# Performance work log

Measured on AMD Instinct MI355X. Metric: run time of the kernel, lower is better.

## Reference

```python
import jax, jax.numpy as jnp
import numpy as np

B, S, D = 4, 512, 2048
N_HEADS, N_KV, HEAD_DIM = 16, 4, 128
N_REP = N_HEADS // N_KV
FFN = 5632
E, TOPK, R = 8, 2, 16
LORA_SCALE = 32.0 / R  # alpha / r
EPS = 1e-5


def setup_inputs() -> dict:
    key = jax.random.key(0)
    ks = jax.random.split(key, 32)

    def p(k, shape, s=0.02):
        return jax.random.normal(k, shape, jnp.float32) * s

    data = jax.random.normal(ks[0], (B, S, D), jnp.float32)
    # causal additive mask [1,1,S,S]
    causal = jnp.tril(jnp.ones((S, S), jnp.bool_))
    mask = jnp.where(causal, 0.0, -1e9).astype(jnp.float32)[None, None]
    # rotary angles (llama interleaved pairing), half head_dim
    inv_freq = 1.0 / (10000.0 ** (np.arange(0, HEAD_DIM, 2, dtype=np.float32) / HEAD_DIM))
    angles = jnp.asarray(np.arange(S, dtype=np.float32)[:, None] * inv_freq[None, :])
    rope_cos = jnp.cos(angles)  # [S, HEAD_DIM//2]
    rope_sin = jnp.sin(angles)

    inp = dict(
        data=data, mask=mask, rope_cos=rope_cos, rope_sin=rope_sin,
        att_norm_w=jnp.ones((D,), jnp.float32),
        ffn_norm_w=jnp.ones((D,), jnp.float32),
        wq=p(ks[1], (D, D)), wk=p(ks[2], (N_KV * HEAD_DIM, D)),
        wv=p(ks[3], (N_KV * HEAD_DIM, D)), wo=p(ks[4], (D, D)),
        lqA=p(ks[5], (R, D)), lqB=p(ks[6], (D, R)),
        lkA=p(ks[7], (R, D)), lkB=p(ks[8], (N_KV * HEAD_DIM, R)),
        lvA=p(ks[9], (R, D)), lvB=p(ks[10], (N_KV * HEAD_DIM, R)),
        loA=p(ks[11], (R, D)), loB=p(ks[12], (D, R)),
        w1=p(ks[13], (FFN, D)), w2=p(ks[14], (D, FFN)), w3=p(ks[15], (FFN, D)),
        gate_w=p(ks[16], (E, D)),
        eA1=p(ks[17], (E, R, D)), eB1=p(ks[18], (E, FFN, R)),
        eA2=p(ks[19], (E, R, FFN)), eB2=p(ks[20], (E, D, R)),
        eA3=p(ks[21], (E, R, D)), eB3=p(ks[22], (E, FFN, R)),
    )
    return inp


def rmsnorm(x, w):
    return x * jax.lax.rsqrt(jnp.mean(x * x, axis=-1, keepdims=True) + EPS) * w


def lora_linear(x, W, A, Bm):
    # torch Linear weight is [out, in]; lora: x @ A^T @ B^T * scale
    return x @ W.T + ((x @ A.T) @ Bm.T) * LORA_SCALE


def apply_rope(x, cos, sin):
    # x: [B,S,H,Dh]; interleaved complex rotation per pair
    x1, x2 = x[..., 0::2], x[..., 1::2]
    c = cos[None, :, None, :]
    s = sin[None, :, None, :]
    o1 = x1 * c - x2 * s
    o2 = x1 * s + x2 * c
    return jnp.stack([o1, o2], axis=-1).reshape(x.shape)


def transformer_fwd(data, mask, rope_cos, rope_sin, att_norm_w, ffn_norm_w,
                    wq, wk, wv, wo, lqA, lqB, lkA, lkB, lvA, lvB, loA, loB,
                    w1, w2, w3, gate_w, eA1, eB1, eA2, eB2, eA3, eB3):
    b, s, _ = data.shape
    h = rmsnorm(data, att_norm_w)
    xq = lora_linear(h, wq, lqA, lqB).reshape(b, s, N_HEADS, HEAD_DIM)
    xk = lora_linear(h, wk, lkA, lkB).reshape(b, s, N_KV, HEAD_DIM)
    xv = lora_linear(h, wv, lvA, lvB).reshape(b, s, N_KV, HEAD_DIM)
    xq = apply_rope(xq, rope_cos, rope_sin)
    xk = apply_rope(xk, rope_cos, rope_sin)
    # repeat_kv: each kv head repeated n_rep times consecutively
    xk = jnp.repeat(xk, N_REP, axis=2)
    xv = jnp.repeat(xv, N_REP, axis=2)
    scores = jnp.einsum('bshd,bthd->bhst', xq, xk) / jnp.sqrt(jnp.float32(HEAD_DIM))
    scores = scores + mask
    attn = jax.nn.softmax(scores, axis=-1)
    out = jnp.einsum('bhst,bthd->bshd', attn, xv).reshape(b, s, D)
    data = data + lora_linear(out, wo, loA, loB)

    # MoE FFN (MixLoRA): shared base w1/w2/w3 + per-expert LoRA, top-k routing
    hn = rmsnorm(data, ffn_norm_w)
    x = hn.reshape(b * s, D)
    logits = x @ gate_w.T                       # [T, E]
    probs = jax.nn.softmax(logits, axis=-1)
    vals, idx = jax.lax.top_k(probs, TOPK)      # [T, k]
    vals = vals / jnp.sum(vals, axis=-1, keepdims=True)
    T = b * s
    route = jnp.zeros((T, E), x.dtype).at[jnp.arange(T)[:, None], idx].set(vals)
    h1 = x @ w1.T   # shared base projections
    h3 = x @ w3.T
    acc = jnp.zeros((T, D), x.dtype)
    for e in range(E):
        g1 = h1 + ((x @ eA1[e].T) @ eB1[e].T) * LORA_SCALE
        g3 = h3 + ((x @ eA3[e].T) @ eB3[e].T) * LORA_SCALE
        gh = jax.nn.silu(g1) * g3
        oe = gh @ w2.T + ((gh @ eA2[e].T) @ eB2[e].T) * LORA_SCALE
        acc = acc + route[:, e:e + 1] * oe
    return data + acc.reshape(b, s, D)


def reference(data, mask, rope_cos, rope_sin, att_norm_w, ffn_norm_w,
              wq, wk, wv, wo, lqA, lqB, lkA, lkB, lvA, lvB, loA, loB,
              w1, w2, w3, gate_w, eA1, eB1, eA2, eB2, eA3, eB3):
    return transformer_fwd(data, mask, rope_cos, rope_sin, att_norm_w, ffn_norm_w,
                           wq, wk, wv, wo, lqA, lqB, lkA, lkB, lvA, lvB, loA, loB,
                           w1, w2, w3, gate_w, eA1, eB1, eA2, eB2, eA3, eB3)
```

## Files before the change

### kernel.cpp

```cpp
#include <hip/hip_runtime.h>
#include <stdint.h>

#define DI static __device__ __forceinline__

typedef __attribute__((ext_vector_type(8))) short bf16x8;
typedef __attribute__((ext_vector_type(4))) float floatx4;

DI unsigned short f2bf(float x){
  unsigned int u = __float_as_uint(x);
  u += 0x7fffu + ((u >> 16) & 1u);
  return (unsigned short)(u >> 16);
}
DI float bf2f(unsigned short h){ return __uint_as_float(((unsigned int)h) << 16); }

#define GLOAD16(gp, lp) \
  __builtin_amdgcn_global_load_lds((const __attribute__((address_space(1))) unsigned int*)(gp), \
                                   (__attribute__((address_space(3))) unsigned int*)(lp), 16, 0, 0)

#define WAITVM0 asm volatile("s_waitcnt vmcnt(0)" ::: "memory")

template<int OUTM, int RESM, bool CSKIP, bool SPLIT>
__global__ __launch_bounds__(256, 2)
void k_gemm(const unsigned short* __restrict__ A, long lda, long sA1, long sA2, long aLo,
            const unsigned short* __restrict__ B, long ldb, long sB1, long sB2, long bLo,
            void* __restrict__ C, long ldc, long sC1, long sC2, long cLo,
            const void* __restrict__ Rz, long ldr,
            const unsigned short* __restrict__ G1p, const float* __restrict__ ewp, int slot,
            int kIters, int zshift, int bshift)
{
  if (CSKIP && blockIdx.y > blockIdx.x) return;
  __shared__ __attribute__((aligned(16))) unsigned short As[SPLIT ? 8192 : 4096];
  __shared__ __attribute__((aligned(16))) unsigned short Bs[SPLIT ? 8192 : 4096];
  const int tid = threadIdx.x;
  const int w = tid >> 6, lane = tid & 63;
  const int wm = (w >> 1) * 64, wn = (w & 1) * 64;
  const int z = blockIdx.z;
  const int zr = z & ((1 << zshift) - 1);
  const int zb = z >> zshift;
  long k0 = 0;
  if (OUTM == 2 || OUTM == 8) k0 = (long)zb * (long)kIters * 32;
  const unsigned short* Ab = A + (long)((OUTM==8)?0:zb) * sA2 + (long)zr * sA1 + (long)blockIdx.x * 128 * lda + k0;
  const unsigned short* Bb = B + (long)((OUTM==8)?0:zb) * sB2 + (long)(zr >> bshift) * sB1 + (long)blockIdx.y * 128 * ldb + k0;

  const int rlo = w * 16 + (lane & 15);
  const int rhi = 64 + rlo;
  const int cc  = (lane >> 4) * 8;
  unsigned short* ldsA0 = As + w * 512;
  unsigned short* ldsA1 = As + 2048 + w * 512;
  unsigned short* ldsB0 = Bs + w * 512;
  unsigned short* ldsB1 = Bs + 2048 + w * 512;

  floatx4 acc[4][4];
  floatx4 zv = {0.f, 0.f, 0.f, 0.f};
#pragma unroll
  for (int i = 0; i < 4; ++i)
#pragma unroll
    for (int j = 0; j < 4; ++j) acc[i][j] = zv;

  const int abase = (wm >> 4) * 512 + lane * 8;
  const int bbase = (wn >> 4) * 512 + lane * 8;

  for (int kt = 0; kt < kIters; ++kt) {
    const unsigned short* pa = Ab + (long)kt * 32;
    const unsigned short* pb = Bb + (long)kt * 32;
    GLOAD16(pa + (long)rlo * lda + cc, ldsA0);
    GLOAD16(pa + (long)rhi * lda + cc, ldsA1);
    GLOAD16(pb + (long)rlo * ldb + cc, ldsB0);
    GLOAD16(pb + (long)rhi * ldb + cc, ldsB1);
    if (SPLIT) {
      const unsigned short* pal = pa + aLo;
      const unsigned short* pbl = pb + bLo;
      GLOAD16(pal + (long)rlo * lda + cc, As + 4096 + w * 512);
      GLOAD16(pal + (long)rhi * lda + cc, As + 6144 + w * 512);
      GLOAD16(pbl + (long)rlo * ldb + cc, Bs + 4096 + w * 512);
      GLOAD16(pbl + (long)rhi * ldb + cc, Bs + 6144 + w * 512);
    }
    __syncthreads();
    bf16x8 af[4], bfr[4];
#pragma unroll
    for (int i = 0; i < 4; ++i)
      af[i] = *(const bf16x8*)(As + abase + i * 512);
#pragma unroll
    for (int j = 0; j < 4; ++j)
      bfr[j] = *(const bf16x8*)(Bs + bbase + j * 512);
    if (SPLIT) {
      bf16x8 al[4], bl[4];
#pragma unroll
      for (int i = 0; i < 4; ++i)
        al[i] = *(const bf16x8*)(As + 4096 + abase + i * 512);
#pragma unroll
      for (int j = 0; j < 4; ++j)
        bl[j] = *(const bf16x8*)(Bs + 4096 + bbase + j * 512);
#pragma unroll
      for (int i = 0; i < 4; ++i)
#pragma unroll
        for (int j = 0; j < 4; ++j) {
          acc[i][j] = __builtin_amdgcn_mfma_f32_16x16x32_bf16(af[i], bfr[j], acc[i][j], 0, 0, 0);
          acc[i][j] = __builtin_amdgcn_mfma_f32_16x16x32_bf16(af[i], bl[j], acc[i][j], 0, 0, 0);
          acc[i][j] = __builtin_amdgcn_mfma_f32_16x16x32_bf16(al[i], bfr[j], acc[i][j], 0, 0, 0);
        }
    } else {
#pragma unroll
      for (int i = 0; i < 4; ++i)
#pragma unroll
        for (int j = 0; j < 4; ++j)
          acc[i][j] = __builtin_amdgcn_mfma_f32_16x16x32_bf16(af[i], bfr[j], acc[i][j], 0, 0, 0);
    }
    __syncthreads();
  }

  const long mb = (long)blockIdx.x * 128 + wm + ((lane >> 4) * 4);
  const long nb = (long)blockIdx.y * 128 + wn + (lane & 15);
  const long cbase = (long)zb * sC2 + (long)zr * sC1;
#pragma unroll
  for (int i = 0; i < 4; ++i) {
#pragma unroll
    for (int j = 0; j < 4; ++j) {
#pragma unroll
      for (int rr = 0; rr < 4; ++rr) {
        long m = mb + i * 16 + rr;
        long n = nb + j * 16;
        float v = acc[i][j][rr];
        if (RESM == 1) v += ((const float*)Rz)[m * ldr + n];
        if (RESM == 2) v += bf2f(((const unsigned short*)Rz)[m * ldr + n]);
        if (OUTM == 0 || OUTM == 8) ((float*)C)[cbase + m * ldc + n] = v;
        else if (OUTM == 1) ((unsigned short*)C)[cbase + m * ldc + n] = f2bf(v);
        else if (OUTM == 2) atomicAdd((float*)C + cbase + m * ldc + n, v);
        else if (OUTM == 4) {
          float g1 = bf2f(G1p[m * ldc + n]);
          float s1 = g1 / (1.f + __expf(-g1));
          ((unsigned short*)C)[cbase + m * ldc + n] = f2bf(ewp[m * 2 + slot] * s1 * v);
        } else if (OUTM == 5) {
          unsigned short h = f2bf(v);
          unsigned short l = f2bf(v - bf2f(h));
          ((unsigned short*)C)[cbase + m * ldc + n] = h;
          ((unsigned short*)C)[cbase + m * ldc + n + cLo] = l;
        } else {
          long bq = m >> 9, sI = m & 511, kv = n >> 7, dI = n & 127;
          long t = (((bq * 4 + kv) * 128 + dI) << 9) + sI;
          unsigned short h = f2bf(v);
          unsigned short l = f2bf(v - bf2f(h));
          ((unsigned short*)C)[t] = h;
          ((unsigned short*)C)[t + cLo] = l;
        }
      }
    }
  }
}

template<int BM, int BN, bool SPLIT, int OUTM, int DEPTH>
__global__ __launch_bounds__(512, 2)
void k_gemm2(const unsigned short* __restrict__ A, long lda, long aLo,
             const unsigned short* __restrict__ B, long ldb, long bLo,
             void* __restrict__ C, long ldc, long sC2, int kIters)
{
  constexpr int ASZ = BM * 32 * (SPLIT ? 2 : 1);
  constexpr int BSZ = BN * 32 * (SPLIT ? 2 : 1);
  constexpr int TSZ = ASZ + BSZ;
  constexpr int FM = BM / 32, FN = BN / 64;
  __shared__ __attribute__((aligned(16))) unsigned short sm[DEPTH * TSZ];

  const int tid = threadIdx.x;
  const int w = tid >> 6, lane = tid & 63;
  const int wm = (w >> 2) * (BM / 2), wn = (w & 3) * (BN / 4);
  const int zb = blockIdx.z;
  const long k0 = (OUTM == 8) ? (long)zb * (long)kIters * 32 : 0;
  const unsigned short* Ab = A + (long)blockIdx.x * BM * lda + k0;
  const unsigned short* Bb = B + (long)blockIdx.y * BN * ldb + k0;
  const int rA = lane & 15;
  const int cc = (lane >> 4) * 8;

  floatx4 acc[FM][FN];
  floatx4 zv = {0.f, 0.f, 0.f, 0.f};
#pragma unroll
  for (int i = 0; i < FM; ++i)
#pragma unroll
    for (int j = 0; j < FN; ++j) acc[i][j] = zv;

  auto stage = [&](int kt) {
    const unsigned short* pa = Ab + (long)kt * 32;
    const unsigned short* pb = Bb + (long)kt * 32;
    unsigned short* sa = sm + (size_t)(kt & (DEPTH - 1)) * TSZ;
    unsigned short* sb = sa + ASZ;
#pragma unroll
    for (int r = 0; r < BM / 128; ++r) {
      const int b = r * 8 + w;
      const long row = b * 16 + rA;
      GLOAD16(pa + row * lda + cc, sa + b * 512);
      if (SPLIT) GLOAD16(pa + aLo + row * lda + cc, sa + BM * 32 + b * 512);
    }
#pragma unroll
    for (int r = 0; r < BN / 128; ++r) {
      const int b = r * 8 + w;
      const long row = b * 16 + rA;
      GLOAD16(pb + row * ldb + cc, sb + b * 512);
      if (SPLIT) GLOAD16(pb + bLo + row * ldb + cc, sb + BN * 32 + b * 512);
    }
  };

  stage(0);
  __builtin_amdgcn_sched_barrier(0);
  WAITVM0;
  __builtin_amdgcn_s_barrier();

  const int aoff = (wm >> 4) * 512 + lane * 8;
  const int boff = (wn >> 4) * 512 + lane * 8;

  for (int kt = 0; kt < kIters; ++kt) {
    if (kt + 1 < kIters) stage(kt + 1);

    const unsigned short* sa = sm + (size_t)(kt & (DEPTH - 1)) * TSZ;
    const unsigned short* sb = sa + ASZ;
    if (SPLIT) {
      bf16x8 bfr[FN], bl[FN];
#pragma unroll
      for (int j = 0; j < FN; ++j) {
        bfr[j] = *(const bf16x8*)(sb + boff + j * 512);
        bl[j]  = *(const bf16x8*)(sb + BN * 32 + boff + j * 512);
      }
      __builtin_amdgcn_s_setprio(1);
#pragma unroll
      for (int i = 0; i < FM; ++i) {
        bf16x8 ai = *(const bf16x8*)(sa + aoff + i * 512);
        bf16x8 ali = *(const bf16x8*)(sa + BM * 32 + aoff + i * 512);
#pragma unroll
        for (int j = 0; j < FN; ++j) {
          acc[i][j] = __builtin_amdgcn_mfma_f32_16x16x32_bf16(ai, bfr[j], acc[i][j], 0, 0, 0);
          acc[i][j] = __builtin_amdgcn_mfma_f32_16x16x32_bf16(ai, bl[j], acc[i][j], 0, 0, 0);
          acc[i][j] = __builtin_amdgcn_mfma_f32_16x16x32_bf16(ali, bfr[j], acc[i][j], 0, 0, 0);
        }
      }
      __builtin_amdgcn_s_setprio(0);
    } else {
      bf16x8 bfr[FN];
#pragma unroll
      for (int j = 0; j < FN; ++j)
        bfr[j] = *(const bf16x8*)(sb + boff + j * 512);
      __builtin_amdgcn_s_setprio(1);
#pragma unroll
      for (int i = 0; i < FM; ++i) {
        bf16x8 ai = *(const bf16x8*)(sa + aoff + i * 512);
#pragma unroll
        for (int j = 0; j < FN; ++j)
          acc[i][j] = __builtin_amdgcn_mfma_f32_16x16x32_bf16(ai, bfr[j], acc[i][j], 0, 0, 0);
      }
      __builtin_amdgcn_s_setprio(0);
    }

    __builtin_amdgcn_sched_barrier(0);
    WAITVM0;
    __builtin_amdgcn_s_barrier();
  }

  const long mb = (long)blockIdx.x * BM + wm + ((lane >> 4) * 4);
  const long nb = (long)blockIdx.y * BN + wn + (lane & 15);
  const long cbase = (long)zb * sC2;
#pragma unroll
  for (int i = 0; i < FM; ++i) {
#pragma unroll
    for (int j = 0; j < FN; ++j) {
#pragma unroll
      for (int rr = 0; rr < 4; ++rr) {
        long m = mb + i * 16 + rr;
        long n = nb + j * 16;
        float v = acc[i][j][rr];
        if (OUTM == 8) ((float*)C)[cbase + m * ldc + n] = v;
        else ((unsigned short*)C)[m * ldc + n] = f2bf(v);
      }
    }
  }
}

__global__ void k_rmsnorm(const float* __restrict__ x, const float* __restrict__ w,
                          unsigned short* __restrict__ ob, long loOff){
  int t = blockIdx.x;
  const float* row = x + (size_t)t * 2048;
  float ss = 0.f;
  for (int i = threadIdx.x; i < 2048; i += 256){ float v = row[i]; ss += v * v; }
#pragma unroll
  for (int o = 32; o; o >>= 1) ss += __shfl_xor(ss, o);
  __shared__ float sred[4]; __shared__ float srms;
  int lane = threadIdx.x & 63, wid = threadIdx.x >> 6;
  if (lane == 0) sred[wid] = ss;
  __syncthreads();
  if (threadIdx.x == 0) srms = rsqrtf((sred[0]+sred[1]+sred[2]+sred[3]) * (1.f/2048.f) + 1e-5f);
  __syncthreads();
  float rr = srms;
  for (int i = threadIdx.x; i < 2048; i += 256){
    float v = row[i] * rr * w[i];
    unsigned short h = f2bf(v);
    ob[(size_t)t * 2048 + i] = h;
    if (loOff) ob[(size_t)t * 2048 + i + loOff] = f2bf(v - bf2f(h));
  }
}

__global__ void k_fold(const float* __restrict__ W, const float* __restrict__ Bm,
                       const float* __restrict__ A, unsigned short* __restrict__ out, long loOff){
  int idx = blockIdx.x * 256 + threadIdx.x;
  int n = idx >> 11, k = idx & 2047;
  float acc = W[idx];
  const float* br = Bm + (size_t)n * 16;
#pragma unroll
  for (int r = 0; r < 16; ++r) acc += 2.0f * br[r] * A[r * 2048 + k];
  unsigned short h = f2bf(acc);
  out[idx] = h;
  out[idx + loOff] = f2bf(acc - bf2f(h));
}

__global__ void k_cvt4(const float* __restrict__ in, unsigned short* __restrict__ out){
  int i = (blockIdx.x * 256 + threadIdx.x) * 4;
  float4 v = *(const float4*)(in + i);
  unsigned long long pk = (unsigned long long)f2bf(v.x)
    | ((unsigned long long)f2bf(v.y) << 16)
    | ((unsigned long long)f2bf(v.z) << 32)
    | ((unsigned long long)f2bf(v.w) << 48);
  *(unsigned long long*)(out + i) = pk;
}

__global__ void k_beff(const float* __restrict__ eB, unsigned short* __restrict__ out, int F){
  int idx = blockIdx.x * 256 + threadIdx.x;
  int f = idx >> 7, er = idx & 127;
  int e = er >> 4, r = er & 15;
  out[idx] = f2bf(eB[((size_t)e * F + f) * 16 + r]);
}

__global__ void k_qkv_epi(const float* __restrict__ P,
                          const float* __restrict__ rc, const float* __restrict__ rs,
                          unsigned short* __restrict__ qb, unsigned short* __restrict__ kb,
                          unsigned short* __restrict__ vT){
  int idx = blockIdx.x * 256 + threadIdx.x;
  int t = idx / 1536, p = idx - t * 1536;
  int c = p * 2;
  const float2 a = *(const float2*)(P + (size_t)t * 3072 + c);
  const float2 b = *(const float2*)(P + 6291456 + (size_t)t * 3072 + c);
  float v0 = a.x + b.x, v1 = a.y + b.y;
  int s = t & 511;
  if (c < 2560) {
    int i = (c & 127) >> 1;
    float co = rc[s * 64 + i], sn = rs[s * 64 + i];
    float o0 = v0 * co - v1 * sn;
    float o1 = v0 * sn + v1 * co;
    v0 = o0; v1 = o1;
  }
  unsigned short h0 = f2bf(v0), l0 = f2bf(v0 - bf2f(h0));
  unsigned short h1 = f2bf(v1), l1 = f2bf(v1 - bf2f(h1));
  if (c < 2048) {
    size_t o = (size_t)t * 2048 + c;
    qb[o] = h0; qb[o + 1] = h1;
    qb[o + 4194304] = l0; qb[o + 4194305] = l1;
  } else if (c < 2560) {
    size_t o = (size_t)t * 512 + (c - 2048);
    kb[o] = h0; kb[o + 1] = h1;
    kb[o + 1048576] = l0; kb[o + 1048577] = l1;
  } else {
    int d = c - 2560;
    int kv = d >> 7, dI = d & 127, bq = t >> 9;
    size_t o = (((size_t)(bq * 4 + kv) * 128 + dI) << 9) + s;
    vT[o] = h0; vT[o + 512] = h1;
    vT[o + 1048576] = l0; vT[o + 1048576 + 512] = l1;
  }
}

__global__ void k_add2res(const float* __restrict__ P, const float* __restrict__ res,
                          float* __restrict__ out){
  int i = (blockIdx.x * 256 + threadIdx.x) * 4;
  float4 a = *(const float4*)(P + i);
  float4 b = *(const float4*)(P + 4194304 + i);
  float4 r = *(const float4*)(res + i);
  float4 o; o.x = a.x + b.x + r.x; o.y = a.y + b.y + r.y;
  o.z = a.z + b.z + r.z; o.w = a.w + b.w + r.w;
  *(float4*)(out + i) = o;
}

__global__ void k_softmax(float* __restrict__ sp){
  int row = blockIdx.x;
  int s = row & 511;
  float* in = sp + (size_t)row * 512;
  unsigned short* op = (unsigned short*)in;
  int t0 = threadIdx.x, t1 = threadIdx.x + 256;
  const float scale = 0.088388347648318447f;
  float v0 = (t0 <= s) ? in[t0] * scale : -3.0e38f;
  float v1 = (t1 <= s) ? in[t1] * scale : -3.0e38f;
  float mx = fmaxf(v0, v1);
#pragma unroll
  for (int o = 32; o; o >>= 1) mx = fmaxf(mx, __shfl_xor(mx, o));
  __shared__ float sred[8];
  int lane = threadIdx.x & 63, wid = threadIdx.x >> 6;
  if (lane == 0) sred[wid] = mx;
  __syncthreads();
  mx = fmaxf(fmaxf(sred[0], sred[1]), fmaxf(sred[2], sred[3]));
  float e0 = (t0 <= s) ? __expf(v0 - mx) : 0.f;
  float e1 = (t1 <= s) ? __expf(v1 - mx) : 0.f;
  float sum = e0 + e1;
#pragma unroll
  for (int o = 32; o; o >>= 1) sum += __shfl_xor(sum, o);
  if (lane == 0) sred[4 + wid] = sum;
  __syncthreads();
  sum = sred[4] + sred[5] + sred[6] + sred[7];
  float inv = 1.f / sum;
  float p0 = e0 * inv, p1 = e1 * inv;
  unsigned short h0 = f2bf(p0), h1 = f2bf(p1);
  op[t0] = h0; op[512 + t0] = f2bf(p0 - bf2f(h0));
  op[t1] = h1; op[512 + t1] = f2bf(p1 - bf2f(h1));
}

__global__ void k_route(const float* __restrict__ x2, const float* __restrict__ w,
                        const float* __restrict__ gw, int* __restrict__ eidx,
                        float* __restrict__ ew){
  int t = blockIdx.x; int lane = threadIdx.x;
  const float* row = x2 + (size_t)t * 2048;
  float ss = 0.f;
  for (int d = lane; d < 2048; d += 64){ float v = row[d]; ss += v * v; }
#pragma unroll
  for (int o = 32; o; o >>= 1) ss += __shfl_xor(ss, o);
  float rr = rsqrtf(ss * (1.f/2048.f) + 1e-5f);
  float acc[8] = {0,0,0,0,0,0,0,0};
  for (int d = lane; d < 2048; d += 64){
    float xv = row[d] * rr * w[d];
#pragma unroll
    for (int e = 0; e < 8; ++e) acc[e] += xv * gw[e * 2048 + d];
  }
#pragma unroll
  for (int e = 0; e < 8; ++e)
#pragma unroll
    for (int o = 32; o; o >>= 1) acc[e] += __shfl_xor(acc[e], o);
  if (lane == 0){
    int i0 = 0;
#pragma unroll
    for (int e = 1; e < 8; ++e) if (acc[e] > acc[i0]) i0 = e;
    int i1 = -1;
#pragma unroll
    for (int e = 0; e < 8; ++e) if (e != i0 && (i1 < 0 || acc[e] > acc[i1])) i1 = e;
    float p1 = __expf(acc[i1] - acc[i0]);
    float inv = 1.f / (1.f + p1);
    eidx[t * 2 + 0] = i0; eidx[t * 2 + 1] = i1;
    ew[t * 2 + 0] = inv;  ew[t * 2 + 1] = p1 * inv;
  }
}

__global__ void k_zero(float* __restrict__ p){
  p[(size_t)blockIdx.x * 256 + threadIdx.x] = 0.f;
}

__global__ void k_ubuild(const float* __restrict__ U1, const float* __restrict__ U3,
                         const int* __restrict__ eidx,
                         unsigned short* __restrict__ u10, unsigned short* __restrict__ u11,
                         unsigned short* __restrict__ u30, unsigned short* __restrict__ u31){
  int idx = blockIdx.x * 256 + threadIdx.x;
  int t = idx >> 7, j = idx & 127; int e = j >> 4;
  int e0 = eidx[t * 2], e1 = eidx[t * 2 + 1];
  float v1 = U1[idx] * 2.0f, v3 = U3[idx] * 2.0f;
  u10[idx] = (e == e0) ? f2bf(v1) : (unsigned short)0;
  u11[idx] = (e == e1) ? f2bf(v1) : (unsigned short)0;
  u30[idx] = (e == e0) ? f2bf(v3) : (unsigned short)0;
  u31[idx] = (e == e1) ? f2bf(v3) : (unsigned short)0;
}

__global__ void k_addip(unsigned short* __restrict__ a, const unsigned short* __restrict__ b){
  size_t i = (size_t)blockIdx.x * 256 + threadIdx.x;
  a[i] = f2bf(bf2f(a[i]) + bf2f(b[i]));
}

__global__ void k_vhat(const float* __restrict__ U20, const float* __restrict__ U21,
                       const int* __restrict__ eidx, unsigned short* __restrict__ out){
  int idx = blockIdx.x * 256 + threadIdx.x;
  int t = idx >> 7, j = idx & 127; int e = j >> 4;
  int e0 = eidx[t * 2], e1 = eidx[t * 2 + 1];
  float v = 0.f;
  if (e == e0) v = 2.0f * U20[idx];
  else if (e == e1) v = 2.0f * U21[idx];
  out[idx] = f2bf(v);
}

extern "C" void kernel_launch(void* const* d_in, const int* in_sizes, int n_in,
                              void* d_out, int out_size, void* d_ws, size_t ws_size,
                              hipStream_t stream){
  const float* data  = (const float*)d_in[0];
  const float* rcos  = (const float*)d_in[2];
  const float* rsin  = (const float*)d_in[3];
  const float* attw  = (const float*)d_in[4];
  const float* ffnw  = (const float*)d_in[5];
  const float* wq    = (const float*)d_in[6];
  const float* wk    = (const float*)d_in[7];
  const float* wv    = (const float*)d_in[8];
  const float* wo    = (const float*)d_in[9];
  const float* lqA   = (const float*)d_in[10];
  const float* lqB   = (const float*)d_in[11];
  const float* lkA   = (const float*)d_in[12];
  const float* lkB   = (const float*)d_in[13];
  const float* lvA   = (const float*)d_in[14];
  const float* lvB   = (const float*)d_in[15];
  const float* loA   = (const float*)d_in[16];
  const float* loB   = (const float*)d_in[17];
  const float* w1    = (const float*)d_in[18];
  const float* w2    = (const float*)d_in[19];
  const float* w3    = (const float*)d_in[20];
  const float* gatew = (const float*)d_in[21];
  const float* eA1   = (const float*)d_in[22];
  const float* eB1   = (const float*)d_in[23];
  const float* eA2   = (const float*)d_in[24];
  const float* eB2   = (const float*)d_in[25];
  const float* eA3   = (const float*)d_in[26];
  const float* eB3   = (const float*)d_in[27];
  (void)in_sizes; (void)n_in; (void)out_size; (void)ws_size;

  char* base = (char*)d_ws;
  float* data2 = (float*)d_out;

  unsigned short* hb   = (unsigned short*)(base + 0);
  unsigned short* Wqkv = (unsigned short*)(base + 16777216);
  float*          QKVf = (float*)(base + 41943040);
  unsigned short* qb   = (unsigned short*)(base + 92274688);
  unsigned short* kb   = (unsigned short*)(base + 109051904);
  unsigned short* vT   = (unsigned short*)(base + 113246208);
  float*          sc   = (float*)(base + 0);
  unsigned short* scU  = (unsigned short*)(base + 0);
  unsigned short* ao   = (unsigned short*)(base + 67108864);
  unsigned short* Wo   = (unsigned short*)(base + 0);
  float*          Wof  = (float*)(base + 16777216);

  size_t off = 0;
  auto alloc = [&](size_t n)->char*{ char* p = base + off; off = (off + n + 255) & ~(size_t)255; return p; };
  int*   eidx = (int*)alloc(16384);
  float* ew   = (float*)alloc(16384);
  unsigned short* hnb  = (unsigned short*)alloc(8388608);
  unsigned short* h1b  = (unsigned short*)alloc(23068672);
  unsigned short* h3b  = (unsigned short*)alloc(23068672);
  unsigned short* wbuf = (unsigned short*)alloc(23068672);
  unsigned short* gh0  = (unsigned short*)alloc(23068672);
  unsigned short* eA1c = (unsigned short*)alloc(524288);
  unsigned short* eA3c = (unsigned short*)alloc(524288);
  unsigned short* eA2c = (unsigned short*)alloc(1441792);
  unsigned short* Bf1  = (unsigned short*)alloc(1441792);
  unsigned short* Bf3  = (unsigned short*)alloc(1441792);
  unsigned short* Bf2  = (unsigned short*)alloc(524288);
  float* Uz = (float*)alloc(4194304);
  float* U1 = Uz, *U3 = Uz + 262144, *U20 = Uz + 524288, *U21 = Uz + 786432;
  unsigned short* Ut10 = (unsigned short*)alloc(524288);
  unsigned short* Ut11 = (unsigned short*)alloc(524288);
  unsigned short* Ut30 = (unsigned short*)alloc(524288);
  unsigned short* Ut31 = (unsigned short*)alloc(524288);
  unsigned short* vhat = (unsigned short*)alloc(524288);
  unsigned short* gh1  = h1b;
  float*          W2f  = (float*)h1b;

  k_rmsnorm<<<2048, 256, 0, stream>>>(data, attw, hb, 4194304);
  k_fold<<<16384, 256, 0, stream>>>(wq, lqB, lqA, Wqkv, 6291456);
  k_fold<<<4096, 256, 0, stream>>>(wk, lkB, lkA, Wqkv + 4194304, 6291456);
  k_fold<<<4096, 256, 0, stream>>>(wv, lvB, lvA, Wqkv + 5242880, 6291456);

  k_gemm2<256,256,true,8,2><<<dim3(8,12,2), 512, 0, stream>>>(
      hb, 2048, 4194304, Wqkv, 2048, 6291456, QKVf, 3072, 6291456, 32);
  k_qkv_epi<<<12288, 256, 0, stream>>>(QKVf, rcos, rsin, qb, kb, vT);

  k_gemm<0,0,true,true><<<dim3(4,4,64), 256, 0, stream>>>(
      qb, 2048, 128, 1048576, 4194304, kb, 512, 128, 262144, 1048576,
      sc, 512, 262144, 4194304, 0, nullptr,0, nullptr,nullptr,0, 4, 4, 2);
  k_softmax<<<32768, 256, 0, stream>>>(sc);
  k_gemm<5,0,false,true><<<dim3(4,1,64), 256, 0, stream>>>(
      scU, 1024, 524288, 8388608, 512, vT, 512, 65536, 262144, 1048576,
      ao, 2048, 128, 1048576, 4194304, nullptr,0, nullptr,nullptr,0, 16, 4, 2);

  k_fold<<<16384, 256, 0, stream>>>(wo, loB, loA, Wo, 4194304);
  k_gemm2<256,128,true,8,2><<<dim3(8,16,2), 512, 0, stream>>>(
      ao, 2048, 4194304, Wo, 2048, 4194304, Wof, 2048, 4194304, 32);
  k_add2res<<<4096, 256, 0, stream>>>(Wof, data, data2);

  k_rmsnorm<<<2048, 256, 0, stream>>>(data2, ffnw, hnb, 0);
  k_route<<<2048, 64, 0, stream>>>(data2, ffnw, gatew, eidx, ew);

  k_cvt4<<<11264, 256, 0, stream>>>(w1, wbuf);
  k_gemm2<256,256,false,1,2><<<dim3(8,22,1), 512, 0, stream>>>(
      hnb, 2048, 0, wbuf, 2048, 0, h1b, 5632, 0, 64);
  k_cvt4<<<11264, 256, 0, stream>>>(w3, wbuf);
  k_gemm2<256,256,false,1,2><<<dim3(8,22,1), 512, 0, stream>>>(
      hnb, 2048, 0, wbuf, 2048, 0, h3b, 5632, 0, 64);

  k_cvt4<<<256, 256, 0, stream>>>(eA1, eA1c);
  k_cvt4<<<256, 256, 0, stream>>>(eA3, eA3c);
  k_cvt4<<<704, 256, 0, stream>>>(eA2, eA2c);
  k_beff<<<2816, 256, 0, stream>>>(eB1, Bf1, 5632);
  k_beff<<<2816, 256, 0, stream>>>(eB3, Bf3, 5632);
  k_beff<<<1024, 256, 0, stream>>>(eB2, Bf2, 2048);
  k_zero<<<4096, 256, 0, stream>>>(Uz);

  k_gemm<2,0,false,false><<<dim3(16,1,8), 256, 0, stream>>>(
      hnb,2048,0,0,0, eA1c,2048,0,0,0, U1,128,0,0,0, nullptr,0, nullptr,nullptr,0, 8,0,0);
  k_gemm<2,0,false,false><<<dim3(16,1,8), 256, 0, stream>>>(
      hnb,2048,0,0,0, eA3c,2048,0,0,0, U3,128,0,0,0, nullptr,0, nullptr,nullptr,0, 8,0,0);
  k_ubuild<<<1024, 256, 0, stream>>>(U1, U3, eidx, Ut10, Ut11, Ut30, Ut31);

  k_gemm<1,2,false,false><<<dim3(16,44,1), 256, 0, stream>>>(
      Ut10,128,0,0,0, Bf1,128,0,0,0, wbuf,5632,0,0,0, h1b,5632, nullptr,nullptr,0, 4,0,0);
  k_gemm<4,2,false,false><<<dim3(16,44,1), 256, 0, stream>>>(
      Ut30,128,0,0,0, Bf3,128,0,0,0, gh0,5632,0,0,0, h3b,5632, wbuf,ew,0, 4,0,0);
  k_gemm<2,0,false,false><<<dim3(16,1,8), 256, 0, stream>>>(
      gh0,5632,0,0,0, eA2c,5632,0,0,0, U20,128,0,0,0, nullptr,0, nullptr,nullptr,0, 22,0,0);
  k_gemm<1,2,false,false><<<dim3(16,44,1), 256, 0, stream>>>(
      Ut11,128,0,0,0, Bf1,128,0,0,0, wbuf,5632,0,0,0, h1b,5632, nullptr,nullptr,0, 4,0,0);
  k_gemm<4,2,false,false><<<dim3(16,44,1), 256, 0, stream>>>(
      Ut31,128,0,0,0, Bf3,128,0,0,0, gh1,5632,0,0,0, h3b,5632, wbuf,ew,1, 4,0,0);
  k_gemm<2,0,false,false><<<dim3(16,1,8), 256, 0, stream>>>(
      gh1,5632,0,0,0, eA2c,5632,0,0,0, U21,128,0,0,0, nullptr,0, nullptr,nullptr,0, 22,0,0);

  k_addip<<<45056, 256, 0, stream>>>(gh0, gh1);
  k_vhat<<<1024, 256, 0, stream>>>(U20, U21, eidx, vhat);
  k_gemm<2,0,false,false><<<dim3(16,16,1), 256, 0, stream>>>(
      vhat,128,0,0,0, Bf2,128,0,0,0, data2,2048,0,0,0, nullptr,0, nullptr,nullptr,0, 4,0,0);
  k_cvt4<<<11264, 256, 0, stream>>>(w2, wbuf);
  k_gemm2<128,256,false,8,2><<<dim3(16,8,2), 512, 0, stream>>>(
      gh0, 5632, 0, wbuf, 5632, 0, W2f, 2048, 4194304, 88);
  k_add2res<<<4096, 256, 0, stream>>>(W2f, data2, data2);
}
```

Before: 1.084 ms.

## Add multi-stage LDS pipeline with partial vmcnt waits to gemm2

Turns the double-buffered k_gemm2 main loop into a ring of DEPTH LDS stages. It now prefetches DEPTH-1 tiles ahead and waits with vmcnt set to the loads still allowed in flight, instead of draining every load each iteration. The Wo, w1/w3 and w2 GEMM launches move to depth 3 or 4, so more global-to-LDS traffic overlaps with MFMA work. In exchange, per-block LDS grows to 96-144KB, which likely leaves room for only one resident block per CU where two fit before.

```diff
diff --git a/kernel.cpp b/kernel.cpp
--- a/kernel.cpp
+++ b/kernel.cpp
@@ -17,7 +17,7 @@
   __builtin_amdgcn_global_load_lds((const __attribute__((address_space(1))) unsigned int*)(gp), \
                                    (__attribute__((address_space(3))) unsigned int*)(lp), 16, 0, 0)
 
-#define WAITVM0 asm volatile("s_waitcnt vmcnt(0)" ::: "memory")
+#define WAITVM(n) asm volatile("s_waitcnt vmcnt(" #n ")" ::: "memory")
 
 template<int OUTM, int RESM, bool CSKIP, bool SPLIT>
 __global__ __launch_bounds__(256, 2)
@@ -158,6 +158,8 @@
   constexpr int BSZ = BN * 32 * (SPLIT ? 2 : 1);
   constexpr int TSZ = ASZ + BSZ;
   constexpr int FM = BM / 32, FN = BN / 64;
+  constexpr int LPT = (SPLIT ? 2 : 1) * (BM / 128 + BN / 128);
+  static_assert(LPT == 3 || LPT == 4 || LPT == 6 || LPT == 8, "vmcnt literals");
   __shared__ __attribute__((aligned(16))) unsigned short sm[DEPTH * TSZ];
 
   const int tid = threadIdx.x;
@@ -177,10 +179,10 @@
 #pragma unroll
     for (int j = 0; j < FN; ++j) acc[i][j] = zv;
 
-  auto stage = [&](int kt) {
+  auto stage = [&](int kt, int sl) {
     const unsigned short* pa = Ab + (long)kt * 32;
     const unsigned short* pb = Bb + (long)kt * 32;
-    unsigned short* sa = sm + (size_t)(kt & (DEPTH - 1)) * TSZ;
+    unsigned short* sa = sm + (size_t)sl * TSZ;
     unsigned short* sb = sa + ASZ;
 #pragma unroll
     for (int r = 0; r < BM / 128; ++r) {
@@ -198,18 +200,32 @@
     }
   };
 
-  stage(0);
+  auto waitpipe = [&](int ahead) {
+    if (ahead <= 0) { WAITVM(0); return; }
+    if (LPT == 3) { if (ahead == 1) { WAITVM(3); } else { WAITVM(6); } }
+    else if (LPT == 4) { if (ahead == 1) { WAITVM(4); } else { WAITVM(8); } }
+    else if (LPT == 6) { if (ahead == 1) { WAITVM(6); } else { WAITVM(12); } }
+    else { if (ahead == 1) { WAITVM(8); } else { WAITVM(16); } }
+  };
+
+  int np = DEPTH - 1; if (np > kIters) np = kIters;
+  for (int p = 0; p < np; ++p) stage(p, p);
   __builtin_amdgcn_sched_barrier(0);
-  WAITVM0;
+  waitpipe(np - 1);
   __builtin_amdgcn_s_barrier();
 
   const int aoff = (wm >> 4) * 512 + lane * 8;
   const int boff = (wn >> 4) * 512 + lane * 8;
 
+  int cs = 0;
+  int ss = (np < DEPTH) ? np : 0;
   for (int kt = 0; kt < kIters; ++kt) {
-    if (kt + 1 < kIters) stage(kt + 1);
-
-    const unsigned short* sa = sm + (size_t)(kt & (DEPTH - 1)) * TSZ;
+    if (kt + DEPTH - 1 < kIters) {
+      stage(kt + DEPTH - 1, ss);
+      ss = (ss + 1 == DEPTH) ? 0 : ss + 1;
+    }
+
+    const unsigned short* sa = sm + (size_t)cs * TSZ;
     const unsigned short* sb = sa + ASZ;
     if (SPLIT) {
       bf16x8 bfr[FN], bl[FN];
@@ -248,8 +264,12 @@
     }
 
     __builtin_amdgcn_sched_barrier(0);
-    WAITVM0;
+    int ahead = kIters - 2 - kt;
+    if (ahead > DEPTH - 2) ahead = DEPTH - 2;
+    if (ahead < 0) ahead = 0;
+    waitpipe(ahead);
     __builtin_amdgcn_s_barrier();
+    cs = (cs + 1 == DEPTH) ? 0 : cs + 1;
   }
 
   const long mb = (long)blockIdx.x * BM + wm + ((lane >> 4) * 4);
@@ -562,7 +582,7 @@
       ao, 2048, 128, 1048576, 4194304, nullptr,0, nullptr,nullptr,0, 16, 4, 2);
 
   k_fold<<<16384, 256, 0, stream>>>(wo, loB, loA, Wo, 4194304);
-  k_gemm2<256,128,true,8,2><<<dim3(8,16,2), 512, 0, stream>>>(
+  k_gemm2<256,128,true,8,3><<<dim3(8,16,2), 512, 0, stream>>>(
       ao, 2048, 4194304, Wo, 2048, 4194304, Wof, 2048, 4194304, 32);
   k_add2res<<<4096, 256, 0, stream>>>(Wof, data, data2);
 
@@ -570,10 +590,10 @@
   k_route<<<2048, 64, 0, stream>>>(data2, ffnw, gatew, eidx, ew);
 
   k_cvt4<<<11264, 256, 0, stream>>>(w1, wbuf);
-  k_gemm2<256,256,false,1,2><<<dim3(8,22,1), 512, 0, stream>>>(
+  k_gemm2<256,256,false,1,4><<<dim3(8,22,1), 512, 0, stream>>>(
       hnb, 2048, 0, wbuf, 2048, 0, h1b, 5632, 0, 64);
   k_cvt4<<<11264, 256, 0, stream>>>(w3, wbuf);
-  k_gemm2<256,256,false,1,2><<<dim3(8,22,1), 512, 0, stream>>>(
+  k_gemm2<256,256,false,1,4><<<dim3(8,22,1), 512, 0, stream>>>(
       hnb, 2048, 0, wbuf, 2048, 0, h3b, 5632, 0, 64);
 
   k_cvt4<<<256, 256, 0, stream>>>(eA1, eA1c);
@@ -608,7 +628,7 @@
   k_gemm<2,0,false,false><<<dim3(16,16,1), 256, 0, stream>>>(
       vhat,128,0,0,0, Bf2,128,0,0,0, data2,2048,0,0,0, nullptr,0, nullptr,nullptr,0, 4,0,0);
   k_cvt4<<<11264, 256, 0, stream>>>(w2, wbuf);
-  k_gemm2<128,256,false,8,2><<<dim3(16,8,2), 512, 0, stream>>>(
+  k_gemm2<128,256,false,8,4><<<dim3(16,8,2), 512, 0, stream>>>(
       gh0, 5632, 0, wbuf, 5632, 0, W2f, 2048, 4194304, 88);
   k_add2res<<<4096, 256, 0, stream>>>(W2f, data2, data2);
 }
```

Result: faster. 1.028 ms (-5.2%).
